# Kernel optimization log

Measured on AMD Instinct MI355X. Metric: run time of the kernel, lower is better.

## Reference

```python
import jax, jax.numpy as jnp
import numpy as np


def _ln(x, g, b, eps=1e-5):
    m = jnp.mean(x, axis=-1, keepdims=True)
    v = jnp.mean((x - m) ** 2, axis=-1, keepdims=True)
    return (x - m) / jnp.sqrt(v + eps) * g + b


def _win_part(x, ws):
    # (B,H,W,C) -> (B*nW, ws*ws, C)
    B, H, W, C = x.shape
    x = x.reshape(B, H // ws, ws, W // ws, ws, C)
    x = jnp.transpose(x, (0, 1, 3, 2, 4, 5))
    return x.reshape(-1, ws * ws, C)


def _win_rev(w, ws, H, W):
    # (B*nW, ws, ws, C) -> (B,H,W,C)
    C = w.shape[-1]
    B = w.shape[0] // ((H // ws) * (W // ws))
    x = w.reshape(B, H // ws, W // ws, ws, ws, C)
    x = jnp.transpose(x, (0, 1, 3, 2, 4, 5))
    return x.reshape(B, H, W, C)


def _build_mask(H, W, ws, ss):
    # standard Swin SW-MSA mask, built with numpy at trace time (static shapes)
    img = np.zeros((H, W), np.float32)
    cnt = 0
    for hs in (slice(0, -ws), slice(-ws, -ss), slice(-ss, None)):
        for wsl in (slice(0, -ws), slice(-ws, -ss), slice(-ss, None)):
            img[hs, wsl] = cnt
            cnt += 1
    mw = img.reshape(H // ws, ws, W // ws, ws).transpose(0, 2, 1, 3).reshape(-1, ws * ws)
    diff = mw[:, None, :] - mw[:, :, None]  # (nW, N, N)
    return jnp.asarray(np.where(diff != 0, -np.inf, 0.0).astype(np.float32))


def _swin_block(x, H, W, ws, shift, heads, p):
    B, L, C = x.shape
    hd = C // heads
    N = ws * ws
    shortcut = x
    xg = _ln(x, p['ln1_g'], p['ln1_b']).reshape(B, H, W, C)
    mask = None
    if shift > 0:
        xg = jnp.roll(xg, shift=(-shift, -shift), axis=(1, 2))
        mask = _build_mask(H, W, ws, shift)
    xw = _win_part(xg, ws)  # (B_, N, C)
    qkv = xw @ p['qkv_w'] + p['qkv_b']  # (B_, N, 3C)
    qkv = jnp.transpose(qkv.reshape(-1, N, 3, heads, hd), (2, 0, 3, 1, 4))
    q, k, v = qkv[0] * (hd ** -0.5), qkv[1], qkv[2]  # (B_, h, N, hd)
    attn = jnp.einsum('bhnd,bhmd->bhnm', q, k)
    if mask is not None:
        nW = mask.shape[0]
        attn = attn.reshape(B, nW, heads, N, N) + mask[None, :, None]
        attn = attn.reshape(-1, heads, N, N)
    attn = jax.nn.softmax(attn, axis=-1)
    out = jnp.einsum('bhnm,bhmd->bhnd', attn, v)
    out = jnp.transpose(out, (0, 2, 1, 3)).reshape(-1, N, C)
    out = out @ p['proj_w'] + p['proj_b']
    xg = _win_rev(out.reshape(-1, ws, ws, C), ws, H, W)
    if shift > 0:
        xg = jnp.roll(xg, shift=(shift, shift), axis=(1, 2))
    x = shortcut + xg.reshape(B, L, C)
    h = jax.nn.gelu(_ln(x, p['ln2_g'], p['ln2_b']) @ p['fc1_w'] + p['fc1_b'], approximate=False)
    return x + (h @ p['fc2_w'] + p['fc2_b'])


def _patch_merge(x, H, W, g, b, w):
    B, L, C = x.shape
    xg = x.reshape(B, H, W, C)
    xc = jnp.concatenate([xg[:, 0::2, 0::2], xg[:, 1::2, 0::2], xg[:, 0::2, 1::2], xg[:, 1::2, 1::2]], axis=-1)
    xc = xc.reshape(B, (H // 2) * (W // 2), 4 * C)
    return _ln(xc, g, b) @ w


def setup_inputs() -> dict:
    key = jax.random.key(0)
    ks = jax.random.split(key, 16)
    B, H, W, C = 8, 96, 96, 128
    s = 0.02
    d = {'x': jax.random.normal(ks[0], (B, H * W, C), jnp.float32)}
    i = 1
    for pre in ('a_', 'b_'):
        d[pre + 'ln1_g'] = jnp.ones((C,), jnp.float32)
        d[pre + 'ln1_b'] = jnp.zeros((C,), jnp.float32)
        d[pre + 'qkv_w'] = s * jax.random.normal(ks[i], (C, 3 * C), jnp.float32); i += 1
        d[pre + 'qkv_b'] = jnp.zeros((3 * C,), jnp.float32)
        d[pre + 'proj_w'] = s * jax.random.normal(ks[i], (C, C), jnp.float32); i += 1
        d[pre + 'proj_b'] = jnp.zeros((C,), jnp.float32)
        d[pre + 'ln2_g'] = jnp.ones((C,), jnp.float32)
        d[pre + 'ln2_b'] = jnp.zeros((C,), jnp.float32)
        d[pre + 'fc1_w'] = s * jax.random.normal(ks[i], (C, 4 * C), jnp.float32); i += 1
        d[pre + 'fc1_b'] = jnp.zeros((4 * C,), jnp.float32)
        d[pre + 'fc2_w'] = s * jax.random.normal(ks[i], (4 * C, C), jnp.float32); i += 1
        d[pre + 'fc2_b'] = jnp.zeros((C,), jnp.float32)
    d['mln_g'] = jnp.ones((4 * C,), jnp.float32)
    d['mln_b'] = jnp.zeros((4 * C,), jnp.float32)
    d['red_w'] = s * jax.random.normal(ks[i], (4 * C, 2 * C), jnp.float32)
    d['H'] = H
    d['W'] = W
    return d


def reference(x, a_ln1_g, a_ln1_b, a_qkv_w, a_qkv_b, a_proj_w, a_proj_b, a_ln2_g, a_ln2_b, a_fc1_w, a_fc1_b, a_fc2_w, a_fc2_b, b_ln1_g, b_ln1_b, b_qkv_w, b_qkv_b, b_proj_w, b_proj_b, b_ln2_g, b_ln2_b, b_fc1_w, b_fc1_b, b_fc2_w, b_fc2_b, mln_g, mln_b, red_w, H, W):
    heads, ws = 4, 8
    pa = dict(ln1_g=a_ln1_g, ln1_b=a_ln1_b, qkv_w=a_qkv_w, qkv_b=a_qkv_b, proj_w=a_proj_w, proj_b=a_proj_b, ln2_g=a_ln2_g, ln2_b=a_ln2_b, fc1_w=a_fc1_w, fc1_b=a_fc1_b, fc2_w=a_fc2_w, fc2_b=a_fc2_b)
    pb = dict(ln1_g=b_ln1_g, ln1_b=b_ln1_b, qkv_w=b_qkv_w, qkv_b=b_qkv_b, proj_w=b_proj_w, proj_b=b_proj_b, ln2_g=b_ln2_g, ln2_b=b_ln2_b, fc1_w=b_fc1_w, fc1_b=b_fc1_b, fc2_w=b_fc2_w, fc2_b=b_fc2_b)
    x = _swin_block(x, H, W, ws, 0, heads, pa)          # W-MSA
    x = _swin_block(x, H, W, ws, ws // 2, heads, pb)     # SW-MSA
    return _patch_merge(x, H, W, mln_g, mln_b, red_w)    # (B, HW/4, 2C)
```

## Files before the change

kernel.cpp:

```cpp
#include <hip/hip_runtime.h>
#include <hip/hip_bf16.h>

typedef __bf16 bf16_t;
typedef __bf16 bf16x2 __attribute__((ext_vector_type(2)));
typedef __bf16 bf16x8 __attribute__((ext_vector_type(8)));
typedef float floatx4 __attribute__((ext_vector_type(4)));

#define NTOK 73728

__device__ __forceinline__ void gl16(const bf16_t* g, bf16_t* l) {
    __builtin_amdgcn_global_load_lds((const __attribute__((address_space(1))) void*)g,
                                     (__attribute__((address_space(3))) void*)l, 16, 0, 0);
}

struct TPack {
    const float* src[9];
    bf16_t* dst[9];
    int K[9], N[9];
};
__global__ __launch_bounds__(256) void kconv_t9(TPack p) {
    int seg = blockIdx.y;
    int K = p.K[seg], N = p.N[seg];
    int idx = blockIdx.x * 256 + threadIdx.x;
    if (idx >= K * N) return;
    int n = idx / K, k = idx - n * K;
    p.dst[seg][idx] = (bf16_t)p.src[seg][k * N + n];
}

__global__ __launch_bounds__(256) void kln128(const float* __restrict__ x, const float* __restrict__ g,
                                              const float* __restrict__ bta, bf16_t* __restrict__ out, int M) {
    int row = blockIdx.x * 4 + (threadIdx.x >> 6);
    int lane = threadIdx.x & 63;
    if (row >= M) return;
    float2 v = *(const float2*)&x[row * 128 + lane * 2];
    float s = v.x + v.y;
    float sq = v.x * v.x + v.y * v.y;
    #pragma unroll
    for (int d = 1; d < 64; d <<= 1) { s += __shfl_xor(s, d, 64); sq += __shfl_xor(sq, d, 64); }
    float m = s * (1.0f / 128.0f);
    float var = sq * (1.0f / 128.0f) - m * m;
    float inv = 1.0f / sqrtf(var + 1e-5f);
    float2 gg = *(const float2*)&g[lane * 2];
    float2 bb = *(const float2*)&bta[lane * 2];
    bf16x2 o;
    o[0] = (bf16_t)((v.x - m) * inv * gg.x + bb.x);
    o[1] = (bf16_t)((v.y - m) * inv * gg.y + bb.y);
    *(bf16x2*)&out[row * 128 + lane * 2] = o;
}

__global__ __launch_bounds__(256) void kmergeln(const float* __restrict__ x, const float* __restrict__ g,
                                                const float* __restrict__ bta, bf16_t* __restrict__ out) {
    int row = blockIdx.x * 4 + (threadIdx.x >> 6);
    int lane = threadIdx.x & 63;
    int b = row / 2304; int rr = row - b * 2304;
    int i2 = rr / 48, j2 = rr - i2 * 48;
    int q = lane >> 4;
    int cc = (lane & 15) * 8;
    int di = q & 1, dj = q >> 1;
    int src = ((b * 96 + i2 * 2 + di) * 96 + (j2 * 2 + dj)) * 128 + cc;
    float4 a0 = *(const float4*)&x[src];
    float4 a1 = *(const float4*)&x[src + 4];
    float s  = a0.x + a0.y + a0.z + a0.w + a1.x + a1.y + a1.z + a1.w;
    float sq = a0.x*a0.x + a0.y*a0.y + a0.z*a0.z + a0.w*a0.w
             + a1.x*a1.x + a1.y*a1.y + a1.z*a1.z + a1.w*a1.w;
    #pragma unroll
    for (int d = 1; d < 64; d <<= 1) { s += __shfl_xor(s, d, 64); sq += __shfl_xor(sq, d, 64); }
    float m = s * (1.0f / 512.0f);
    float var = sq * (1.0f / 512.0f) - m * m;
    float inv = 1.0f / sqrtf(var + 1e-5f);
    int c = q * 128 + cc;
    float4 g0 = *(const float4*)&g[c];
    float4 g1 = *(const float4*)&g[c + 4];
    float4 b0 = *(const float4*)&bta[c];
    float4 b1 = *(const float4*)&bta[c + 4];
    bf16x8 o;
    o[0] = (bf16_t)((a0.x - m) * inv * g0.x + b0.x);
    o[1] = (bf16_t)((a0.y - m) * inv * g0.y + b0.y);
    o[2] = (bf16_t)((a0.z - m) * inv * g0.z + b0.z);
    o[3] = (bf16_t)((a0.w - m) * inv * g0.w + b0.w);
    o[4] = (bf16_t)((a1.x - m) * inv * g1.x + b1.x);
    o[5] = (bf16_t)((a1.y - m) * inv * g1.y + b1.y);
    o[6] = (bf16_t)((a1.z - m) * inv * g1.z + b1.z);
    o[7] = (bf16_t)((a1.w - m) * inv * g1.w + b1.w);
    *(bf16x8*)&out[row * 512 + c] = o;
}

template<int MODE>
__global__ __launch_bounds__(256) void gemm128(const bf16_t* __restrict__ A,
                                               const bf16_t* __restrict__ Bt,
                                               const float* __restrict__ bias,
                                               const float* __restrict__ res,
                                               float* __restrict__ outf,
                                               bf16_t* __restrict__ outh,
                                               int M, int N, int K) {
    alignas(16) __shared__ bf16_t lA[128 * 32];
    alignas(16) __shared__ bf16_t lB[128 * 32];
    const int tid = threadIdx.x;
    const int lane = tid & 63;
    const int wv = tid >> 6;
    const int wm = (wv & 1) * 64, wn = (wv >> 1) * 64;
    const int frow = lane & 15, fq = lane >> 4;
    const int rowA = blockIdx.y * 128;
    const int rowB = blockIdx.x * 128;
    const int srow = tid >> 2, scol = (tid & 3) * 8;
    const bf16_t* pa = A + (size_t)(rowA + srow) * K + scol;
    const bf16_t* pb = Bt + (size_t)(rowB + srow) * K + scol;
    const size_t half = (size_t)64 * K;
    floatx4 acc[4][4] = {};
    for (int k0 = 0; k0 < K; k0 += 32) {
        __syncthreads();
        gl16(pa + k0,        &lA[tid * 8]);
        gl16(pa + half + k0, &lA[2048 + tid * 8]);
        gl16(pb + k0,        &lB[tid * 8]);
        gl16(pb + half + k0, &lB[2048 + tid * 8]);
        __syncthreads();
        bf16x8 af[4], bfr[4];
        #pragma unroll
        for (int i = 0; i < 4; i++) {
            af[i]  = *(const bf16x8*)&lA[(wm + i * 16 + frow) * 32 + fq * 8];
            bfr[i] = *(const bf16x8*)&lB[(wn + i * 16 + frow) * 32 + fq * 8];
        }
        #pragma unroll
        for (int i = 0; i < 4; i++)
            #pragma unroll
            for (int j = 0; j < 4; j++)
                acc[i][j] = __builtin_amdgcn_mfma_f32_16x16x32_bf16(af[i], bfr[j], acc[i][j], 0, 0, 0);
    }
    #pragma unroll
    for (int i = 0; i < 4; i++) {
        #pragma unroll
        for (int j = 0; j < 4; j++) {
            int col = rowB + wn + j * 16 + frow;
            float bs = (MODE == 3) ? 0.0f : bias[col];
            #pragma unroll
            for (int r = 0; r < 4; r++) {
                int row = rowA + wm + i * 16 + fq * 4 + r;
                float v = acc[i][j][r] + bs;
                size_t off = (size_t)row * N + col;
                if (MODE == 0) {
                    outh[off] = (bf16_t)v;
                } else if (MODE == 1) {
                    outf[off] = res[off] + v;
                } else if (MODE == 2) {
                    outh[off] = (bf16_t)(0.5f * v * (1.0f + erff(v * 0.70710678118654752f)));
                } else {
                    outf[off] = v;
                }
            }
        }
    }
}

__global__ __launch_bounds__(64) void kattn(const bf16_t* __restrict__ qkv, bf16_t* __restrict__ out, int shift) {
    alignas(16) __shared__ bf16_t lp[64 * 64];
    alignas(16) __shared__ bf16_t lv[64 * 32];
    int blk = blockIdx.x;
    int win = blk >> 2, h = blk & 3;
    int b = win / 144; int wr = win - b * 144;
    int wi = wr / 12, wj = wr - wi * 12;
    int ri0 = wi * 8, rj0 = wj * 8;
    int lane = threadIdx.x;
    auto trow = [&](int n) {
        int oi = ri0 + (n >> 3) + shift; oi = (oi >= 96) ? oi - 96 : oi;
        int oj = rj0 + (n & 7) + shift;  oj = (oj >= 96) ? oj - 96 : oj;
        return (b * 96 + oi) * 96 + oj;
    };
    {
        size_t base = (size_t)trow(lane) * 384 + 256 + h * 32;
        *(uint4*)&lv[lane * 32]      = *(const uint4*)&qkv[base];
        *(uint4*)&lv[lane * 32 + 8]  = *(const uint4*)&qkv[base + 8];
        *(uint4*)&lv[lane * 32 + 16] = *(const uint4*)&qkv[base + 16];
        *(uint4*)&lv[lane * 32 + 24] = *(const uint4*)&qkv[base + 24];
    }
    int frow = lane & 15, fk = (lane >> 4) * 8;
    bf16x8 qf[4], kf[4];
    #pragma unroll
    for (int t = 0; t < 4; t++) {
        size_t rq = (size_t)trow(t * 16 + frow) * 384;
        qf[t] = *(const bf16x8*)&qkv[rq + h * 32 + fk];
        kf[t] = *(const bf16x8*)&qkv[rq + 128 + h * 32 + fk];
    }
    floatx4 S[4][4] = {};
    #pragma unroll
    for (int mt = 0; mt < 4; mt++)
        #pragma unroll
        for (int nt = 0; nt < 4; nt++)
            S[mt][nt] = __builtin_amdgcn_mfma_f32_16x16x32_bf16(qf[mt], kf[nt], S[mt][nt], 0, 0, 0);
    const float scale = 0.17677669529663687f;
    #pragma unroll
    for (int mt = 0; mt < 4; mt++)
        #pragma unroll
        for (int nt = 0; nt < 4; nt++)
            #pragma unroll
            for (int r = 0; r < 4; r++) S[mt][nt][r] *= scale;
    if (shift > 0) {
        auto grpn = [&](int n) {
            int ri = ri0 + (n >> 3), rj = rj0 + (n & 7);
            int gr = (ri < 88) ? 0 : ((ri < 92) ? 1 : 2);
            int gc = (rj < 88) ? 0 : ((rj < 92) ? 1 : 2);
            return gr * 3 + gc;
        };
        int gk[4];
        #pragma unroll
        for (int nt = 0; nt < 4; nt++) gk[nt] = grpn(nt * 16 + frow);
        #pragma unroll
        for (int mt = 0; mt < 4; mt++)
            #pragma unroll
            for (int r = 0; r < 4; r++) {
                int gq = grpn(mt * 16 + (lane >> 4) * 4 + r);
                #pragma unroll
                for (int nt = 0; nt < 4; nt++)
                    if (gq != gk[nt]) S[mt][nt][r] = -1e30f;
            }
    }
    #pragma unroll
    for (int mt = 0; mt < 4; mt++) {
        #pragma unroll
        for (int r = 0; r < 4; r++) {
            float mx = fmaxf(fmaxf(S[mt][0][r], S[mt][1][r]), fmaxf(S[mt][2][r], S[mt][3][r]));
            #pragma unroll
            for (int d = 1; d < 16; d <<= 1) mx = fmaxf(mx, __shfl_xor(mx, d, 64));
            float sm = 0.0f;
            #pragma unroll
            for (int nt = 0; nt < 4; nt++) {
                float p = __expf(S[mt][nt][r] - mx);
                S[mt][nt][r] = p;
                sm += p;
            }
            #pragma unroll
            for (int d = 1; d < 16; d <<= 1) sm += __shfl_xor(sm, d, 64);
            float inv = 1.0f / sm;
            #pragma unroll
            for (int nt = 0; nt < 4; nt++) S[mt][nt][r] *= inv;
        }
    }
    #pragma unroll
    for (int mt = 0; mt < 4; mt++)
        #pragma unroll
        for (int nt = 0; nt < 4; nt++)
            #pragma unroll
            for (int r = 0; r < 4; r++)
                lp[(mt * 16 + (lane >> 4) * 4 + r) * 64 + nt * 16 + frow] = (bf16_t)S[mt][nt][r];
    __syncthreads();
    floatx4 O[4][2] = {};
    #pragma unroll
    for (int ks = 0; ks < 2; ks++) {
        bf16x8 vbs[2];
        #pragma unroll
        for (int nt = 0; nt < 2; nt++)
            #pragma unroll
            for (int j = 0; j < 8; j++)
                vbs[nt][j] = lv[(ks * 32 + fk + j) * 32 + nt * 16 + frow];
        #pragma unroll
        for (int mt = 0; mt < 4; mt++) {
            bf16x8 pa = *(const bf16x8*)&lp[(mt * 16 + frow) * 64 + ks * 32 + fk];
            #pragma unroll
            for (int nt = 0; nt < 2; nt++)
                O[mt][nt] = __builtin_amdgcn_mfma_f32_16x16x32_bf16(pa, vbs[nt], O[mt][nt], 0, 0, 0);
        }
    }
    #pragma unroll
    for (int mt = 0; mt < 4; mt++) {
        #pragma unroll
        for (int r = 0; r < 4; r++) {
            int qr = mt * 16 + (lane >> 4) * 4 + r;
            size_t orow = (size_t)trow(qr) * 128 + h * 32;
            #pragma unroll
            for (int nt = 0; nt < 2; nt++)
                out[orow + nt * 16 + frow] = (bf16_t)O[mt][nt][r];
        }
    }
}

extern "C" void kernel_launch(void* const* d_in, const int* in_sizes, int n_in,
                              void* d_out, int out_size, void* d_ws, size_t ws_size,
                              hipStream_t stream) {
    const float* x       = (const float*)d_in[0];
    const float* a_ln1g  = (const float*)d_in[1];
    const float* a_ln1b  = (const float*)d_in[2];
    const float* a_qkvw  = (const float*)d_in[3];
    const float* a_qkvb  = (const float*)d_in[4];
    const float* a_projw = (const float*)d_in[5];
    const float* a_projb = (const float*)d_in[6];
    const float* a_ln2g  = (const float*)d_in[7];
    const float* a_ln2b  = (const float*)d_in[8];
    const float* a_fc1w  = (const float*)d_in[9];
    const float* a_fc1b  = (const float*)d_in[10];
    const float* a_fc2w  = (const float*)d_in[11];
    const float* a_fc2b  = (const float*)d_in[12];
    const float* b_ln1g  = (const float*)d_in[13];
    const float* b_ln1b  = (const float*)d_in[14];
    const float* b_qkvw  = (const float*)d_in[15];
    const float* b_qkvb  = (const float*)d_in[16];
    const float* b_projw = (const float*)d_in[17];
    const float* b_projb = (const float*)d_in[18];
    const float* b_ln2g  = (const float*)d_in[19];
    const float* b_ln2b  = (const float*)d_in[20];
    const float* b_fc1w  = (const float*)d_in[21];
    const float* b_fc1b  = (const float*)d_in[22];
    const float* b_fc2w  = (const float*)d_in[23];
    const float* b_fc2b  = (const float*)d_in[24];
    const float* mlng    = (const float*)d_in[25];
    const float* mlnb    = (const float*)d_in[26];
    const float* redw    = (const float*)d_in[27];
    float* out = (float*)d_out;

    char* p = (char*)d_ws;
    float*  buf_x   = (float*)p;  p += (size_t)NTOK * 128 * 4;
    bf16_t* buf_ln  = (bf16_t*)p; p += (size_t)NTOK * 128 * 2;
    bf16_t* buf_big = (bf16_t*)p; p += (size_t)NTOK * 512 * 2;
    bf16_t* wt      = (bf16_t*)p;
    bf16_t* buf_qkv  = buf_big;
    bf16_t* buf_attn = buf_big + (size_t)NTOK * 384;
    bf16_t* aqkvT  = wt;
    bf16_t* aprojT = aqkvT  + 384 * 128;
    bf16_t* afc1T  = aprojT + 128 * 128;
    bf16_t* afc2T  = afc1T  + 512 * 128;
    bf16_t* bqkvT  = afc2T  + 128 * 512;
    bf16_t* bprojT = bqkvT  + 384 * 128;
    bf16_t* bfc1T  = bprojT + 128 * 128;
    bf16_t* bfc2T  = bfc1T  + 512 * 128;
    bf16_t* redT   = bfc2T  + 128 * 512;

    TPack tp;
    const float* srcs[9] = {a_qkvw, a_projw, a_fc1w, a_fc2w, b_qkvw, b_projw, b_fc1w, b_fc2w, redw};
    bf16_t* dsts[9] = {aqkvT, aprojT, afc1T, afc2T, bqkvT, bprojT, bfc1T, bfc2T, redT};
    int Ks[9] = {128, 128, 128, 512, 128, 128, 128, 512, 512};
    int Ns[9] = {384, 128, 512, 128, 384, 128, 512, 128, 256};
    for (int i = 0; i < 9; i++) { tp.src[i] = srcs[i]; tp.dst[i] = dsts[i]; tp.K[i] = Ks[i]; tp.N[i] = Ns[i]; }
    kconv_t9<<<dim3(512, 9), dim3(256), 0, stream>>>(tp);

    const dim3 blk256(256);
    const int MG = NTOK / 128;

    kln128<<<dim3(NTOK / 4), blk256, 0, stream>>>(x, a_ln1g, a_ln1b, buf_ln, NTOK);
    gemm128<0><<<dim3(3, MG), blk256, 0, stream>>>(buf_ln, aqkvT, a_qkvb, nullptr, nullptr, buf_qkv, NTOK, 384, 128);
    kattn<<<dim3(1152 * 4), dim3(64), 0, stream>>>(buf_qkv, buf_attn, 0);
    gemm128<1><<<dim3(1, MG), blk256, 0, stream>>>(buf_attn, aprojT, a_projb, x, buf_x, nullptr, NTOK, 128, 128);
    kln128<<<dim3(NTOK / 4), blk256, 0, stream>>>(buf_x, a_ln2g, a_ln2b, buf_ln, NTOK);
    gemm128<2><<<dim3(4, MG), blk256, 0, stream>>>(buf_ln, afc1T, a_fc1b, nullptr, nullptr, buf_big, NTOK, 512, 128);
    gemm128<1><<<dim3(1, MG), blk256, 0, stream>>>(buf_big, afc2T, a_fc2b, buf_x, buf_x, nullptr, NTOK, 128, 512);

    kln128<<<dim3(NTOK / 4), blk256, 0, stream>>>(buf_x, b_ln1g, b_ln1b, buf_ln, NTOK);
    gemm128<0><<<dim3(3, MG), blk256, 0, stream>>>(buf_ln, bqkvT, b_qkvb, nullptr, nullptr, buf_qkv, NTOK, 384, 128);
    kattn<<<dim3(1152 * 4), dim3(64), 0, stream>>>(buf_qkv, buf_attn, 4);
    gemm128<1><<<dim3(1, MG), blk256, 0, stream>>>(buf_attn, bprojT, b_projb, buf_x, buf_x, nullptr, NTOK, 128, 128);
    kln128<<<dim3(NTOK / 4), blk256, 0, stream>>>(buf_x, b_ln2g, b_ln2b, buf_ln, NTOK);
    gemm128<2><<<dim3(4, MG), blk256, 0, stream>>>(buf_ln, bfc1T, b_fc1b, nullptr, nullptr, buf_big, NTOK, 512, 128);
    gemm128<1><<<dim3(1, MG), blk256, 0, stream>>>(buf_big, bfc2T, b_fc2b, buf_x, buf_x, nullptr, NTOK, 128, 512);

    kmergeln<<<dim3(18432 / 4), blk256, 0, stream>>>(buf_x, mlng, mlnb, buf_big);
    gemm128<3><<<dim3(2, 144), blk256, 0, stream>>>(buf_big, redT, nullptr, nullptr, out, nullptr, 18432, 256, 512);
}
```

Measured before the change: 496.6 us.

## Use 64x128 GEMM tiles with K=64 steps and tanh-form GELU

Replaces the 128x128 GEMM tile with a 64x128 tile that loads K in chunks of 64, which halves the number of barrier pairs per K loop and doubles the block count. An occupancy hint of 5 blocks per CU is added. The GELU epilogue swaps erff for a tanh approximation written as a sigmoid with __expf, cutting transcendental cost at some accuracy risk. Smaller M tiles reduce reuse of the B tile, and the grid sizes are adjusted to match.

```diff
diff --git a/kernel.cpp b/kernel.cpp
--- a/kernel.cpp
+++ b/kernel.cpp
@@ -86,48 +86,55 @@
 }
 
 template<int MODE>
-__global__ __launch_bounds__(256) void gemm128(const bf16_t* __restrict__ A,
-                                               const bf16_t* __restrict__ Bt,
-                                               const float* __restrict__ bias,
-                                               const float* __restrict__ res,
-                                               float* __restrict__ outf,
-                                               bf16_t* __restrict__ outh,
-                                               int M, int N, int K) {
-    alignas(16) __shared__ bf16_t lA[128 * 32];
-    alignas(16) __shared__ bf16_t lB[128 * 32];
+__global__ __launch_bounds__(256, 5) void gemm64x128(const bf16_t* __restrict__ A,
+                                                     const bf16_t* __restrict__ Bt,
+                                                     const float* __restrict__ bias,
+                                                     const float* __restrict__ res,
+                                                     float* __restrict__ outf,
+                                                     bf16_t* __restrict__ outh,
+                                                     int M, int N, int K) {
+    alignas(16) __shared__ bf16_t lA[2 * 64 * 32];
+    alignas(16) __shared__ bf16_t lB[2 * 128 * 32];
     const int tid = threadIdx.x;
     const int lane = tid & 63;
     const int wv = tid >> 6;
-    const int wm = (wv & 1) * 64, wn = (wv >> 1) * 64;
+    const int wm = (wv & 1) * 32;
+    const int wn = (wv >> 1) * 64;
     const int frow = lane & 15, fq = lane >> 4;
-    const int rowA = blockIdx.y * 128;
+    const int rowA = blockIdx.y * 64;
     const int rowB = blockIdx.x * 128;
-    const int srow = tid >> 2, scol = (tid & 3) * 8;
-    const bf16_t* pa = A + (size_t)(rowA + srow) * K + scol;
-    const bf16_t* pb = Bt + (size_t)(rowB + srow) * K + scol;
-    const size_t half = (size_t)64 * K;
-    floatx4 acc[4][4] = {};
-    for (int k0 = 0; k0 < K; k0 += 32) {
+    const int sr = tid >> 2, sc = (tid & 3) * 8;
+    const bf16_t* pa = A + (size_t)(rowA + sr) * K + sc;
+    const bf16_t* pb0 = Bt + (size_t)(rowB + sr) * K + sc;
+    const bf16_t* pb1 = Bt + (size_t)(rowB + 64 + sr) * K + sc;
+    floatx4 acc[2][4] = {};
+    for (int k0 = 0; k0 < K; k0 += 64) {
         __syncthreads();
-        gl16(pa + k0,        &lA[tid * 8]);
-        gl16(pa + half + k0, &lA[2048 + tid * 8]);
-        gl16(pb + k0,        &lB[tid * 8]);
-        gl16(pb + half + k0, &lB[2048 + tid * 8]);
+        gl16(pa  + k0,      &lA[tid * 8]);
+        gl16(pa  + k0 + 32, &lA[2048 + tid * 8]);
+        gl16(pb0 + k0,      &lB[tid * 8]);
+        gl16(pb1 + k0,      &lB[2048 + tid * 8]);
+        gl16(pb0 + k0 + 32, &lB[4096 + tid * 8]);
+        gl16(pb1 + k0 + 32, &lB[4096 + 2048 + tid * 8]);
         __syncthreads();
-        bf16x8 af[4], bfr[4];
-        #pragma unroll
-        for (int i = 0; i < 4; i++) {
-            af[i]  = *(const bf16x8*)&lA[(wm + i * 16 + frow) * 32 + fq * 8];
-            bfr[i] = *(const bf16x8*)&lB[(wn + i * 16 + frow) * 32 + fq * 8];
-        }
-        #pragma unroll
-        for (int i = 0; i < 4; i++)
+        #pragma unroll
+        for (int s = 0; s < 2; s++) {
+            bf16x8 af[2], bfr[4];
+            #pragma unroll
+            for (int i = 0; i < 2; i++)
+                af[i] = *(const bf16x8*)&lA[s * 2048 + (wm + i * 16 + frow) * 32 + fq * 8];
             #pragma unroll
             for (int j = 0; j < 4; j++)
-                acc[i][j] = __builtin_amdgcn_mfma_f32_16x16x32_bf16(af[i], bfr[j], acc[i][j], 0, 0, 0);
-    }
-    #pragma unroll
-    for (int i = 0; i < 4; i++) {
+                bfr[j] = *(const bf16x8*)&lB[s * 4096 + (wn + j * 16 + frow) * 32 + fq * 8];
+            #pragma unroll
+            for (int i = 0; i < 2; i++)
+                #pragma unroll
+                for (int j = 0; j < 4; j++)
+                    acc[i][j] = __builtin_amdgcn_mfma_f32_16x16x32_bf16(af[i], bfr[j], acc[i][j], 0, 0, 0);
+        }
+    }
+    #pragma unroll
+    for (int i = 0; i < 2; i++) {
         #pragma unroll
         for (int j = 0; j < 4; j++) {
             int col = rowB + wn + j * 16 + frow;
@@ -142,7 +149,8 @@
                 } else if (MODE == 1) {
                     outf[off] = res[off] + v;
                 } else if (MODE == 2) {
-                    outh[off] = (bf16_t)(0.5f * v * (1.0f + erff(v * 0.70710678118654752f)));
+                    float u = 1.5957691216057308f * (v + 0.044715f * v * v * v);
+                    outh[off] = (bf16_t)(v / (1.0f + __expf(-u)));
                 } else {
                     outf[off] = v;
                 }
@@ -331,24 +339,24 @@
     kconv_t9<<<dim3(512, 9), dim3(256), 0, stream>>>(tp);
 
     const dim3 blk256(256);
-    const int MG = NTOK / 128;
+    const int MG = NTOK / 64;
 
     kln128<<<dim3(NTOK / 4), blk256, 0, stream>>>(x, a_ln1g, a_ln1b, buf_ln, NTOK);
-    gemm128<0><<<dim3(3, MG), blk256, 0, stream>>>(buf_ln, aqkvT, a_qkvb, nullptr, nullptr, buf_qkv, NTOK, 384, 128);
+    gemm64x128<0><<<dim3(3, MG), blk256, 0, stream>>>(buf_ln, aqkvT, a_qkvb, nullptr, nullptr, buf_qkv, NTOK, 384, 128);
     kattn<<<dim3(1152 * 4), dim3(64), 0, stream>>>(buf_qkv, buf_attn, 0);
-    gemm128<1><<<dim3(1, MG), blk256, 0, stream>>>(buf_attn, aprojT, a_projb, x, buf_x, nullptr, NTOK, 128, 128);
+    gemm64x128<1><<<dim3(1, MG), blk256, 0, stream>>>(buf_attn, aprojT, a_projb, x, buf_x, nullptr, NTOK, 128, 128);
     kln128<<<dim3(NTOK / 4), blk256, 0, stream>>>(buf_x, a_ln2g, a_ln2b, buf_ln, NTOK);
-    gemm128<2><<<dim3(4, MG), blk256, 0, stream>>>(buf_ln, afc1T, a_fc1b, nullptr, nullptr, buf_big, NTOK, 512, 128);
-    gemm128<1><<<dim3(1, MG), blk256, 0, stream>>>(buf_big, afc2T, a_fc2b, buf_x, buf_x, nullptr, NTOK, 128, 512);
+    gemm64x128<2><<<dim3(4, MG), blk256, 0, stream>>>(buf_ln, afc1T, a_fc1b, nullptr, nullptr, buf_big, NTOK, 512, 128);
+    gemm64x128<1><<<dim3(1, MG), blk256, 0, stream>>>(buf_big, afc2T, a_fc2b, buf_x, buf_x, nullptr, NTOK, 128, 512);
 
     kln128<<<dim3(NTOK / 4), blk256, 0, stream>>>(buf_x, b_ln1g, b_ln1b, buf_ln, NTOK);
-    gemm128<0><<<dim3(3, MG), blk256, 0, stream>>>(buf_ln, bqkvT, b_qkvb, nullptr, nullptr, buf_qkv, NTOK, 384, 128);
+    gemm64x128<0><<<dim3(3, MG), blk256, 0, stream>>>(buf_ln, bqkvT, b_qkvb, nullptr, nullptr, buf_qkv, NTOK, 384, 128);
     kattn<<<dim3(1152 * 4), dim3(64), 0, stream>>>(buf_qkv, buf_attn, 4);
-    gemm128<1><<<dim3(1, MG), blk256, 0, stream>>>(buf_attn, bprojT, b_projb, buf_x, buf_x, nullptr, NTOK, 128, 128);
+    gemm64x128<1><<<dim3(1, MG), blk256, 0, stream>>>(buf_attn, bprojT, b_projb, buf_x, buf_x, nullptr, NTOK, 128, 128);
     kln128<<<dim3(NTOK / 4), blk256, 0, stream>>>(buf_x, b_ln2g, b_ln2b, buf_ln, NTOK);
-    gemm128<2><<<dim3(4, MG), blk256, 0, stream>>>(buf_ln, bfc1T, b_fc1b, nullptr, nullptr, buf_big, NTOK, 512, 128);
-    gemm128<1><<<dim3(1, MG), blk256, 0, stream>>>(buf_big, bfc2T, b_fc2b, buf_x, buf_x, nullptr, NTOK, 128, 512);
+    gemm64x128<2><<<dim3(4, MG), blk256, 0, stream>>>(buf_ln, bfc1T, b_fc1b, nullptr, nullptr, buf_big, NTOK, 512, 128);
+    gemm64x128<1><<<dim3(1, MG), blk256, 0, stream>>>(buf_big, bfc2T, b_fc2b, buf_x, buf_x, nullptr, NTOK, 128, 512);
 
     kmergeln<<<dim3(18432 / 4), blk256, 0, stream>>>(buf_x, mlng, mlnb, buf_big);
-    gemm128<3><<<dim3(2, 144), blk256, 0, stream>>>(buf_big, redT, nullptr, nullptr, out, nullptr, 18432, 256, 512);
-}
+    gemm64x128<3><<<dim3(2, 288), blk256, 0, stream>>>(buf_big, redT, nullptr, nullptr, out, nullptr, 18432, 256, 512);
+}
```

Result: faster. 460.6 us (-7.2%).
